# Kernel tuning notes

Measured on AMD Instinct MI355X. Metric: run time of the kernel, lower is better.

## Reference

```python
import jax, jax.numpy as jnp
import numpy as np

P_DROP = 0.2
NEG_SLOPE = 0.2


def setup_inputs() -> dict:
    key = jax.random.key(0)
    ks = jax.random.split(key, 12)
    N, E = 50000, 800000
    IN, H1, H2, OUT = 256, 256, 128, 64
    x = jax.random.normal(ks[0], (N, IN), dtype=jnp.float32)
    adj_rows = jax.random.randint(ks[1], (E,), 0, N, dtype=jnp.int32)
    adj_cols = jax.random.randint(ks[2], (E,), 0, N, dtype=jnp.int32)
    adj_vals = jax.random.uniform(ks[3], (E,), dtype=jnp.float32)
    W1 = jax.random.normal(ks[4], (H1, IN), dtype=jnp.float32) * (1.0 / np.sqrt(IN))
    b1 = jax.random.normal(ks[5], (H1,), dtype=jnp.float32) * 0.01
    W2 = jax.random.normal(ks[6], (H2, H1), dtype=jnp.float32) * (1.0 / np.sqrt(H1))
    b2 = jax.random.normal(ks[7], (H2,), dtype=jnp.float32) * 0.01
    W3 = jax.random.normal(ks[8], (OUT, H2), dtype=jnp.float32) * (1.0 / np.sqrt(H2))
    b3 = jax.random.normal(ks[9], (OUT,), dtype=jnp.float32) * 0.01
    mask1 = jax.random.bernoulli(ks[10], 1.0 - P_DROP, (N, H1))
    mask2 = jax.random.bernoulli(ks[11], 1.0 - P_DROP, (N, H2))
    return {"x": x, "adj_rows": adj_rows, "adj_cols": adj_cols, "adj_vals": adj_vals,
            "W1": W1, "b1": b1, "W2": W2, "b2": b2, "W3": W3, "b3": b3,
            "mask1": mask1, "mask2": mask2}


def _spmm(rows, cols, vals, h, n_nodes):
    # sparse adjacency matmul: out[r] = sum_e vals[e] * h[cols[e]] for rows[e]==r
    msgs = vals[:, None] * h[cols]  # [E, d] irregular gather
    return jax.ops.segment_sum(msgs, rows, num_segments=n_nodes)


def _gcn_layer(x, W, b, rows, cols, vals, n_nodes):
    h = x @ W.T + b  # nn.Linear
    return _spmm(rows, cols, vals, h, n_nodes)


def reference(x, adj_rows, adj_cols, adj_vals, W1, b1, W2, b2, W3, b3, mask1, mask2):
    N = x.shape[0]
    keep = 1.0 / (1.0 - P_DROP)
    h = _gcn_layer(x, W1, b1, adj_rows, adj_cols, adj_vals, N)
    h = jnp.where(h >= 0, h, NEG_SLOPE * h)
    h = jnp.where(mask1, h * keep, 0.0)
    h = _gcn_layer(h, W2, b2, adj_rows, adj_cols, adj_vals, N)
    h = jnp.where(h >= 0, h, NEG_SLOPE * h)
    h = jnp.where(mask2, h * keep, 0.0)
    z = _gcn_layer(h, W3, b3, adj_rows, adj_cols, adj_vals, N)
    return z
```

## Files before the change

kernel.cpp:

```cpp
#include <hip/hip_runtime.h>


typedef unsigned short ushort_t;
typedef __attribute__((ext_vector_type(8))) short bf16x8;
typedef __attribute__((ext_vector_type(4))) float f32x4;
typedef __attribute__((ext_vector_type(2))) unsigned int u32x2;

__device__ __forceinline__ float bf2f(ushort_t u) {
  return __uint_as_float(((unsigned int)u) << 16);
}
__device__ __forceinline__ ushort_t f2bf(float f) {
  unsigned int u = __float_as_uint(f);
  return (ushort_t)((u + 0x7FFFu + ((u >> 16) & 1u)) >> 16);
}
__device__ __forceinline__ float read_f(const void* p, int fm, size_t i) {
  return fm ? bf2f(((const ushort_t*)p)[i]) : ((const float*)p)[i];
}

__device__ __forceinline__ size_t frag_off(int m, int k, int K) {
  return (size_t)(m >> 4) * 16 * K + ((size_t)(k >> 5) << 9) +
         (((k >> 3) & 3) << 7) + ((m & 15) << 3) + (k & 7);
}

__device__ __forceinline__ bool mask_keep(const void* mask, int mm, size_t o) {
  switch (mm) {
    case 1:  return ((const int*)mask)[o] != 0;
    case 2:  return ((const unsigned int*)mask)[o] != 0u;
    case 3:  return ((const ushort_t*)mask)[o] != 0;
    default: return ((const unsigned char*)mask)[o] != 0;
  }
}

__global__ void prep_kernel(const void* __restrict__ x,
                            const void* __restrict__ m1,
                            const void* __restrict__ m2,
                            int* __restrict__ modes,
                            int* __restrict__ zero_region, int zn) {
  if (blockIdx.x == 0) {
    __shared__ int bfok;
    if (threadIdx.x == 0) bfok = 1;
    __syncthreads();
    for (int i = threadIdx.x; i < 8192; i += blockDim.x) {
      ushort_t h = ((const ushort_t*)x)[i];
      int e = (h >> 7) & 0xFF;
      if (!(h == 0 || (e >= 95 && e <= 133))) atomicAnd(&bfok, 0);
    }
    __syncthreads();
    if (threadIdx.x == 0) modes[0] = bfok;
  } else if (blockIdx.x <= 2) {
    const void* p = (blockIdx.x == 1) ? m1 : m2;
    __shared__ int ok[4];
    if (threadIdx.x < 4) ok[threadIdx.x] = 1;
    __syncthreads();
    for (int i = threadIdx.x; i < 4096; i += blockDim.x) {
      unsigned int w = ((const unsigned int*)p)[i];
      if (!(w == 0u || w == 1u)) atomicAnd(&ok[0], 0);
      if (!(w == 0u || w == 0x3F800000u)) atomicAnd(&ok[1], 0);
      unsigned int h16 = w >> 16, l16 = w & 0xFFFFu;
      if (!((h16 == 0u || h16 == 0x3F80u) && (l16 == 0u || l16 == 0x3F80u)))
        atomicAnd(&ok[2], 0);
      if (((w | (w >> 8) | (w >> 16) | (w >> 24)) & 0xFEu) != 0u) atomicAnd(&ok[3], 0);
    }
    __syncthreads();
    if (threadIdx.x == 0)
      modes[blockIdx.x] = ok[0] ? 1 : (ok[1] ? 2 : (ok[2] ? 3 : 0));
  } else {
    int i = (blockIdx.x - 3) * blockDim.x + threadIdx.x;
    int stride = (gridDim.x - 3) * blockDim.x;
    for (; i < zn; i += stride) zero_region[i] = 0;
  }
}

__global__ void hist_kernel(const int* __restrict__ rows, int* __restrict__ cnt, int E) {
  int i = blockIdx.x * blockDim.x + threadIdx.x;
  int stride = gridDim.x * blockDim.x;
  for (; i < E; i += stride) atomicAdd(&cnt[rows[i]], 1);
}

__global__ void scan_part_kernel(const int* __restrict__ cnt, int* __restrict__ part, int n) {
  __shared__ int s[256];
  int i = blockIdx.x * 256 + threadIdx.x;
  s[threadIdx.x] = (i < n) ? cnt[i] : 0;
  __syncthreads();
  for (int off = 128; off > 0; off >>= 1) {
    if (threadIdx.x < off) s[threadIdx.x] += s[threadIdx.x + off];
    __syncthreads();
  }
  if (threadIdx.x == 0) part[blockIdx.x] = s[0];
}

__global__ __launch_bounds__(1024) void scan_top_kernel(int* __restrict__ part, int P) {
  __shared__ int s[1024];
  int t = threadIdx.x;
  int v = (t < P) ? part[t] : 0;
  s[t] = v;
  __syncthreads();
  for (int off = 1; off < 1024; off <<= 1) {
    int x = s[t];
    int y = (t >= off) ? s[t - off] : 0;
    __syncthreads();
    s[t] = x + y;
    __syncthreads();
  }
  if (t < P) part[t] = s[t] - v;
}

__global__ void scan_apply_kernel(const int* __restrict__ cnt, const int* __restrict__ part,
                                  int* __restrict__ row_start, int n) {
  __shared__ int s[256];
  int base = part[blockIdx.x];
  int i = blockIdx.x * 256 + threadIdx.x;
  int v = (i < n) ? cnt[i] : 0;
  s[threadIdx.x] = v;
  __syncthreads();
  for (int off = 1; off < 256; off <<= 1) {
    int x = s[threadIdx.x];
    int y = (threadIdx.x >= off) ? s[threadIdx.x - off] : 0;
    __syncthreads();
    s[threadIdx.x] = x + y;
    __syncthreads();
  }
  if (i < n) row_start[i] = base + s[threadIdx.x] - v;
  if (i == n - 1) row_start[n] = base + s[threadIdx.x];
}

__global__ void scatter_kernel(const int* __restrict__ rows, const int* __restrict__ cols,
                               const void* __restrict__ vals, const int* __restrict__ fm_p,
                               const int* __restrict__ row_start, int* __restrict__ fill,
                               int2* __restrict__ ecv, int E) {
  int fm = *fm_p;
  int i = blockIdx.x * blockDim.x + threadIdx.x;
  int stride = gridDim.x * blockDim.x;
  for (; i < E; i += stride) {
    int r = rows[i];
    int pos = atomicAdd(&fill[r], 1);
    int idx = row_start[r] + pos;
    ecv[idx] = make_int2(cols[i], __float_as_int(read_f(vals, fm, i)));
  }
}

__global__ void convert_all_kernel(
    const void* __restrict__ W1, const void* __restrict__ W2, const void* __restrict__ W3,
    const void* __restrict__ b1, const void* __restrict__ b2, const void* __restrict__ b3,
    const void* __restrict__ x, const int* __restrict__ fm_p,
    ushort_t* __restrict__ whi, ushort_t* __restrict__ wlo,
    float* __restrict__ biasf, ushort_t* __restrict__ xbf,
    int n1, int n2, int n3, int h1, int h2, int h3, int K1, int K2, int K3, int nx) {
  int fm = *fm_p;
  int wtot = n1 + n2 + n3;
  int btot = h1 + h2 + h3;
  int nx4 = nx / 4;
  int total = wtot + btot + nx4;
  int i = blockIdx.x * blockDim.x + threadIdx.x;
  int stride = gridDim.x * blockDim.x;
  for (; i < total; i += stride) {
    if (i < wtot) {
      const void* src; int j, K; size_t base;
      if (i < n1) { src = W1; j = i; K = K1; base = 0; }
      else if (i < n1 + n2) { src = W2; j = i - n1; K = K2; base = n1; }
      else { src = W3; j = i - n1 - n2; K = K3; base = (size_t)n1 + n2; }
      int n = j / K, k = j - n * K;
      float v = read_f(src, fm, j);
      ushort_t h = f2bf(v);
      size_t o = base + frag_off(n, k, K);
      whi[o] = h;
      wlo[o] = f2bf(v - bf2f(h));
    } else if (i < wtot + btot) {
      int k = i - wtot;
      const void* src; int j;
      if (k < h1) { src = b1; j = k; }
      else if (k < h1 + h2) { src = b2; j = k - h1; }
      else { src = b3; j = k - h1 - h2; }
      biasf[k] = read_f(src, fm, j);
    } else {
      int k4 = i - wtot - btot;
      int m = k4 / (K1 / 4);
      int k0 = (k4 - m * (K1 / 4)) * 4;
      ushort_t p0, p1, p2, p3;
      if (fm == 0) {
        f32x4 v = ((const f32x4*)x)[k4];
        p0 = f2bf(v[0]); p1 = f2bf(v[1]); p2 = f2bf(v[2]); p3 = f2bf(v[3]);
      } else {
        const ushort_t* xb = (const ushort_t*)x + (size_t)k4 * 4;
        p0 = xb[0]; p1 = xb[1]; p2 = xb[2]; p3 = xb[3];
      }
      size_t o = frag_off(m, k0, K1);
      *(u32x2*)(xbf + o) = (u32x2){
          (unsigned int)p0 | ((unsigned int)p1 << 16),
          (unsigned int)p2 | ((unsigned int)p3 << 16)};
    }
  }
}

template<int KC>
__global__ __launch_bounds__(256) void gemm_breg_kernel(
    const ushort_t* __restrict__ A,
    const ushort_t* __restrict__ Whi, const ushort_t* __restrict__ Wlo,
    const float* __restrict__ bias, ushort_t* __restrict__ g, int ldg,
    int M, int nct) {
  const int K = KC * 32;
  int wave = threadIdx.x >> 6, lane = threadIdx.x & 63;
  int gw = blockIdx.x * 4 + wave;
  int NW = gridDim.x * 4;
  int mr = lane & 15, quad = lane >> 4;
  int ct = gw % nct;
  int nrt = (M + 15) >> 4;
  int ntasks = nct * nrt;
  if (gw >= ntasks) return;

  bf16x8 wh[KC], wl[KC];
  {
    const ushort_t* wp = Whi + (size_t)ct * 16 * K + lane * 8;
    const ushort_t* wq = Wlo + (size_t)ct * 16 * K + lane * 8;
#pragma unroll
    for (int kc = 0; kc < KC; ++kc) {
      wh[kc] = *(const bf16x8*)(wp + kc * 512);
      wl[kc] = *(const bf16x8*)(wq + kc * 512);
    }
  }
  int col = ct * 16 + mr;
  float bv = bias[col];

  int task = gw;
  bf16x8 af[KC];
  {
    const ushort_t* ap = A + (size_t)(task / nct) * 16 * K + lane * 8;
#pragma unroll
    for (int kc = 0; kc < KC; ++kc) af[kc] = *(const bf16x8*)(ap + kc * 512);
  }

#pragma unroll 1
  for (;;) {
    int next = task + NW;
    bool has_next = next < ntasks;
    bf16x8 afn[KC];
    if (has_next) {
      const ushort_t* ap = A + (size_t)(next / nct) * 16 * K + lane * 8;
#pragma unroll
      for (int kc = 0; kc < KC; ++kc) afn[kc] = *(const bf16x8*)(ap + kc * 512);
    }

    f32x4 acc[4];
#pragma unroll
    for (int t = 0; t < 4; ++t) acc[t] = (f32x4){0.f, 0.f, 0.f, 0.f};
#pragma unroll
    for (int kc = 0; kc < KC; ++kc) {
      acc[(2 * kc) & 3] = __builtin_amdgcn_mfma_f32_16x16x32_bf16(af[kc], wh[kc], acc[(2 * kc) & 3], 0, 0, 0);
      acc[(2 * kc + 1) & 3] = __builtin_amdgcn_mfma_f32_16x16x32_bf16(af[kc], wl[kc], acc[(2 * kc + 1) & 3], 0, 0, 0);
    }
    int m0 = (task / nct) * 16;
#pragma unroll
    for (int r = 0; r < 4; ++r) {
      int row = m0 + quad * 4 + r;
      float s = ((acc[0][r] + acc[1][r]) + (acc[2][r] + acc[3][r])) + bv;
      if (row < M) g[(size_t)row * ldg + col] = f2bf(s);
    }
    if (!has_next) break;
#pragma unroll
    for (int kc = 0; kc < KC; ++kc) af[kc] = afn[kc];
    task = next;
  }
}

template<int MODE, int VEC>
__global__ __launch_bounds__(256) void spmm7_kernel(
    const int* __restrict__ row_start, const int2* __restrict__ ecv,
    const ushort_t* __restrict__ G, int D,
    const void* __restrict__ mask, const int* __restrict__ mmode_p,
    void* __restrict__ outp, int N) {
  int wave = threadIdx.x >> 6, lane = threadIdx.x & 63;
  int r = blockIdx.x * 4 + wave;
  if (r >= N) return;
  int f0 = lane * VEC;
  int e  = __builtin_amdgcn_readfirstlane(row_start[r]);
  int e1 = __builtin_amdgcn_readfirstlane(row_start[r + 1]);
  float a[VEC];
#pragma unroll
  for (int q = 0; q < VEC; ++q) a[q] = 0.f;

  for (; e + 8 <= e1; e += 8) {
    int2 cv[8];
#pragma unroll
    for (int j = 0; j < 8; ++j) cv[j] = ecv[e + j];
    if (VEC == 4) {
      u32x2 gg[8];
#pragma unroll
      for (int j = 0; j < 8; ++j)
        gg[j] = *(const u32x2*)(G + (size_t)cv[j].x * D + f0);
#pragma unroll
      for (int j = 0; j < 8; ++j) {
        float v = __int_as_float(cv[j].y);
        a[0] += v * bf2f((ushort_t)gg[j][0]);
        a[1] += v * bf2f((ushort_t)(gg[j][0] >> 16));
        a[2] += v * bf2f((ushort_t)gg[j][1]);
        a[3] += v * bf2f((ushort_t)(gg[j][1] >> 16));
      }
    } else if (VEC == 2) {
      unsigned int gg[8];
#pragma unroll
      for (int j = 0; j < 8; ++j)
        gg[j] = *(const unsigned int*)(G + (size_t)cv[j].x * D + f0);
#pragma unroll
      for (int j = 0; j < 8; ++j) {
        float v = __int_as_float(cv[j].y);
        a[0] += v * bf2f((ushort_t)gg[j]);
        a[1] += v * bf2f((ushort_t)(gg[j] >> 16));
      }
    } else {
      ushort_t h[8];
#pragma unroll
      for (int j = 0; j < 8; ++j) h[j] = G[(size_t)cv[j].x * D + f0];
#pragma unroll
      for (int j = 0; j < 8; ++j) a[0] += __int_as_float(cv[j].y) * bf2f(h[j]);
    }
  }
  if (e < e1) {
    int idx[8]; float v[8];
#pragma unroll
    for (int j = 0; j < 8; ++j) {
      int ee = e + j;
      bool ok = ee < e1;
      int2 cv = ecv[ok ? ee : e1 - 1];
      idx[j] = cv.x;
      v[j] = ok ? __int_as_float(cv.y) : 0.f;
    }
    if (VEC == 4) {
      u32x2 gg[8];
#pragma unroll
      for (int j = 0; j < 8; ++j)
        gg[j] = *(const u32x2*)(G + (size_t)idx[j] * D + f0);
#pragma unroll
      for (int j = 0; j < 8; ++j) {
        a[0] += v[j] * bf2f((ushort_t)gg[j][0]);
        a[1] += v[j] * bf2f((ushort_t)(gg[j][0] >> 16));
        a[2] += v[j] * bf2f((ushort_t)gg[j][1]);
        a[3] += v[j] * bf2f((ushort_t)(gg[j][1] >> 16));
      }
    } else if (VEC == 2) {
      unsigned int gg[8];
#pragma unroll
      for (int j = 0; j < 8; ++j)
        gg[j] = *(const unsigned int*)(G + (size_t)idx[j] * D + f0);
#pragma unroll
      for (int j = 0; j < 8; ++j) {
        a[0] += v[j] * bf2f((ushort_t)gg[j]);
        a[1] += v[j] * bf2f((ushort_t)(gg[j] >> 16));
      }
    } else {
      ushort_t h[8];
#pragma unroll
      for (int j = 0; j < 8; ++j) h[j] = G[(size_t)idx[j] * D + f0];
#pragma unroll
      for (int j = 0; j < 8; ++j) a[0] += v[j] * bf2f(h[j]);
    }
  }

  if (MODE == 1) {
    size_t om = (size_t)r * D + f0;
    int mm = *mmode_p;
    ushort_t pk[VEC];
#pragma unroll
    for (int q = 0; q < VEC; ++q) {
      float t = a[q];
      t = (t >= 0.f) ? t : 0.2f * t;
      t = mask_keep(mask, mm, om + q) ? t * 1.25f : 0.f;
      pk[q] = f2bf(t);
    }
    size_t o = frag_off(r, f0, D);
    if (VEC == 4) {
      *(u32x2*)((ushort_t*)outp + o) = (u32x2){
          (unsigned int)pk[0] | ((unsigned int)pk[1] << 16),
          (unsigned int)pk[2] | ((unsigned int)pk[3] << 16)};
    } else if (VEC == 2) {
      *(unsigned int*)((ushort_t*)outp + o) =
          (unsigned int)pk[0] | ((unsigned int)pk[1] << 16);
    } else {
      ((ushort_t*)outp)[o] = pk[0];
    }
  } else {
    size_t o = (size_t)r * D + f0;
#pragma unroll
    for (int q = 0; q < VEC; ++q) ((float*)outp)[o + q] = a[q];
  }
}

extern "C" void kernel_launch(void* const* d_in, const int* in_sizes, int n_in,
                              void* d_out, int out_size, void* d_ws, size_t ws_size,
                              hipStream_t stream) {
  const void* x     = d_in[0];
  const int*  rows  = (const int*)d_in[1];
  const int*  cols  = (const int*)d_in[2];
  const void* vals  = d_in[3];
  const void* W1    = d_in[4];
  const void* b1    = d_in[5];
  const void* W2    = d_in[6];
  const void* b2    = d_in[7];
  const void* W3    = d_in[8];
  const void* b3    = d_in[9];
  const void* mask1 = d_in[10];
  const void* mask2 = d_in[11];

  const int H1  = in_sizes[5];
  const int H2  = in_sizes[7];
  const int OUT = in_sizes[9];
  const int IN  = in_sizes[4] / H1;
  const int N   = in_sizes[0] / IN;
  const int E   = in_sizes[1];
  const int W1n = in_sizes[4], W2n = in_sizes[6], W3n = in_sizes[8];
  const int Np  = ((N + 15) / 16) * 16;

  char* ws = (char*)d_ws;
  size_t off = 0;
  auto alloc = [&](size_t bytes) -> void* {
    void* p = ws + off;
    off = (off + bytes + 255) & ~(size_t)255;
    return p;
  };
  int*      modes     = (int*)alloc(4 * 4);
  int*      row_start = (int*)alloc((size_t)(N + 1) * 4);
  int*      cnt       = (int*)alloc((size_t)N * 8);
  int*      part      = (int*)alloc(1024 * 4);
  int2*     ecv       = (int2*)alloc((size_t)E * 8);
  ushort_t* whi       = (ushort_t*)alloc((size_t)(W1n + W2n + W3n) * 2);
  ushort_t* wlo       = (ushort_t*)alloc((size_t)(W1n + W2n + W3n) * 2);
  float*    biasf     = (float*)alloc((size_t)(H1 + H2 + OUT) * 4);
  ushort_t* bufA      = (ushort_t*)alloc((size_t)Np * H1 * 2);
  ushort_t* bufB      = (ushort_t*)alloc((size_t)Np * H1 * 2);
  ushort_t* bufC      = (ushort_t*)alloc((size_t)Np * H1 * 2);

  int* fmode = modes;
  int* mm1   = modes + 1;
  int* mm2   = modes + 2;
  int* fill  = cnt + N;
  ushort_t* w1hi = whi,             *w1lo = wlo;
  ushort_t* w2hi = whi + W1n,       *w2lo = wlo + W1n;
  ushort_t* w3hi = whi + W1n + W2n, *w3lo = wlo + W1n + W2n;

  prep_kernel<<<259, 256, 0, stream>>>(x, mask1, mask2, modes, cnt, 2 * N);

  const int P = (N + 255) / 256;
  hist_kernel<<<1024, 256, 0, stream>>>(rows, cnt, E);
  scan_part_kernel<<<P, 256, 0, stream>>>(cnt, part, N);
  scan_top_kernel<<<1, 1024, 0, stream>>>(part, P);
  scan_apply_kernel<<<P, 256, 0, stream>>>(cnt, part, row_start, N);
  scatter_kernel<<<1024, 256, 0, stream>>>(rows, cols, vals, fmode, row_start, fill, ecv, E);

  convert_all_kernel<<<2048, 256, 0, stream>>>(
      W1, W2, W3, b1, b2, b3, x, fmode, whi, wlo, biasf, bufA,
      W1n, W2n, W3n, H1, H2, OUT, IN, H1, H2, N * IN);

  const int GEMM_BLOCKS = 1024;
  int spmm_grid = (N + 3) / 4;

  gemm_breg_kernel<8><<<GEMM_BLOCKS, 256, 0, stream>>>(
      bufA, w1hi, w1lo, biasf, bufB, H1, N, H1 / 16);
  spmm7_kernel<1, 4><<<spmm_grid, 256, 0, stream>>>(
      row_start, ecv, bufB, H1, mask1, mm1, bufC, N);
  gemm_breg_kernel<8><<<GEMM_BLOCKS, 256, 0, stream>>>(
      bufC, w2hi, w2lo, biasf + H1, bufB, H2, N, H2 / 16);
  spmm7_kernel<1, 2><<<spmm_grid, 256, 0, stream>>>(
      row_start, ecv, bufB, H2, mask2, mm2, bufA, N);
  gemm_breg_kernel<4><<<GEMM_BLOCKS, 256, 0, stream>>>(
      bufA, w3hi, w3lo, biasf + H1 + H2, bufB, OUT, N, OUT / 16);
  spmm7_kernel<0, 1><<<spmm_grid, 256, 0, stream>>>(
      row_start, ecv, bufB, OUT, nullptr, fmode, d_out, N);
}
```

Measured before the change: 454.0 us.

## Merge scatter and convert kernels; vectorize mask loads and stage SpMM fragment stores

```diff
diff --git a/kernel.cpp b/kernel.cpp
--- a/kernel.cpp
+++ b/kernel.cpp
@@ -5,6 +5,7 @@
 typedef __attribute__((ext_vector_type(8))) short bf16x8;
 typedef __attribute__((ext_vector_type(4))) float f32x4;
 typedef __attribute__((ext_vector_type(2))) unsigned int u32x2;
+typedef __attribute__((ext_vector_type(4))) unsigned int u32x4;
 
 __device__ __forceinline__ float bf2f(ushort_t u) {
   return __uint_as_float(((unsigned int)u) << 16);
@@ -124,70 +125,70 @@
   if (i == n - 1) row_start[n] = base + s[threadIdx.x];
 }
 
-__global__ void scatter_kernel(const int* __restrict__ rows, const int* __restrict__ cols,
-                               const void* __restrict__ vals, const int* __restrict__ fm_p,
-                               const int* __restrict__ row_start, int* __restrict__ fill,
-                               int2* __restrict__ ecv, int E) {
-  int fm = *fm_p;
-  int i = blockIdx.x * blockDim.x + threadIdx.x;
-  int stride = gridDim.x * blockDim.x;
-  for (; i < E; i += stride) {
-    int r = rows[i];
-    int pos = atomicAdd(&fill[r], 1);
-    int idx = row_start[r] + pos;
-    ecv[idx] = make_int2(cols[i], __float_as_int(read_f(vals, fm, i)));
-  }
-}
-
-__global__ void convert_all_kernel(
+__global__ void scatter_convert_kernel(
+    const int* __restrict__ rows, const int* __restrict__ cols,
+    const void* __restrict__ vals, const int* __restrict__ fm_p,
+    const int* __restrict__ row_start, int* __restrict__ fill,
+    int2* __restrict__ ecv, int E,
     const void* __restrict__ W1, const void* __restrict__ W2, const void* __restrict__ W3,
     const void* __restrict__ b1, const void* __restrict__ b2, const void* __restrict__ b3,
-    const void* __restrict__ x, const int* __restrict__ fm_p,
+    const void* __restrict__ x,
     ushort_t* __restrict__ whi, ushort_t* __restrict__ wlo,
     float* __restrict__ biasf, ushort_t* __restrict__ xbf,
     int n1, int n2, int n3, int h1, int h2, int h3, int K1, int K2, int K3, int nx) {
   int fm = *fm_p;
-  int wtot = n1 + n2 + n3;
-  int btot = h1 + h2 + h3;
-  int nx4 = nx / 4;
-  int total = wtot + btot + nx4;
-  int i = blockIdx.x * blockDim.x + threadIdx.x;
-  int stride = gridDim.x * blockDim.x;
-  for (; i < total; i += stride) {
-    if (i < wtot) {
-      const void* src; int j, K; size_t base;
-      if (i < n1) { src = W1; j = i; K = K1; base = 0; }
-      else if (i < n1 + n2) { src = W2; j = i - n1; K = K2; base = n1; }
-      else { src = W3; j = i - n1 - n2; K = K3; base = (size_t)n1 + n2; }
-      int n = j / K, k = j - n * K;
-      float v = read_f(src, fm, j);
-      ushort_t h = f2bf(v);
-      size_t o = base + frag_off(n, k, K);
-      whi[o] = h;
-      wlo[o] = f2bf(v - bf2f(h));
-    } else if (i < wtot + btot) {
-      int k = i - wtot;
-      const void* src; int j;
-      if (k < h1) { src = b1; j = k; }
-      else if (k < h1 + h2) { src = b2; j = k - h1; }
-      else { src = b3; j = k - h1 - h2; }
-      biasf[k] = read_f(src, fm, j);
-    } else {
-      int k4 = i - wtot - btot;
-      int m = k4 / (K1 / 4);
-      int k0 = (k4 - m * (K1 / 4)) * 4;
-      ushort_t p0, p1, p2, p3;
-      if (fm == 0) {
-        f32x4 v = ((const f32x4*)x)[k4];
-        p0 = f2bf(v[0]); p1 = f2bf(v[1]); p2 = f2bf(v[2]); p3 = f2bf(v[3]);
+  if (blockIdx.x < 1024) {
+    int i = blockIdx.x * blockDim.x + threadIdx.x;
+    int stride = 1024 * blockDim.x;
+    for (; i < E; i += stride) {
+      int r = rows[i];
+      int pos = atomicAdd(&fill[r], 1);
+      int idx = row_start[r] + pos;
+      ecv[idx] = make_int2(cols[i], __float_as_int(read_f(vals, fm, i)));
+    }
+  } else {
+    int wtot = n1 + n2 + n3;
+    int btot = h1 + h2 + h3;
+    int nx4 = nx / 4;
+    int total = wtot + btot + nx4;
+    int i = (blockIdx.x - 1024) * blockDim.x + threadIdx.x;
+    int stride = (gridDim.x - 1024) * blockDim.x;
+    for (; i < total; i += stride) {
+      if (i < wtot) {
+        const void* src; int j, K; size_t base;
+        if (i < n1) { src = W1; j = i; K = K1; base = 0; }
+        else if (i < n1 + n2) { src = W2; j = i - n1; K = K2; base = n1; }
+        else { src = W3; j = i - n1 - n2; K = K3; base = (size_t)n1 + n2; }
+        int n = j / K, k = j - n * K;
+        float v = read_f(src, fm, j);
+        ushort_t h = f2bf(v);
+        size_t o = base + frag_off(n, k, K);
+        whi[o] = h;
+        wlo[o] = f2bf(v - bf2f(h));
+      } else if (i < wtot + btot) {
+        int k = i - wtot;
+        const void* src; int j;
+        if (k < h1) { src = b1; j = k; }
+        else if (k < h1 + h2) { src = b2; j = k - h1; }
+        else { src = b3; j = k - h1 - h2; }
+        biasf[k] = read_f(src, fm, j);
       } else {
-        const ushort_t* xb = (const ushort_t*)x + (size_t)k4 * 4;
-        p0 = xb[0]; p1 = xb[1]; p2 = xb[2]; p3 = xb[3];
-      }
-      size_t o = frag_off(m, k0, K1);
-      *(u32x2*)(xbf + o) = (u32x2){
-          (unsigned int)p0 | ((unsigned int)p1 << 16),
-          (unsigned int)p2 | ((unsigned int)p3 << 16)};
+        int k4 = i - wtot - btot;
+        int m = k4 / (K1 / 4);
+        int k0 = (k4 - m * (K1 / 4)) * 4;
+        ushort_t p0, p1, p2, p3;
+        if (fm == 0) {
+          f32x4 v = ((const f32x4*)x)[k4];
+          p0 = f2bf(v[0]); p1 = f2bf(v[1]); p2 = f2bf(v[2]); p3 = f2bf(v[3]);
+        } else {
+          const ushort_t* xb = (const ushort_t*)x + (size_t)k4 * 4;
+          p0 = xb[0]; p1 = xb[1]; p2 = xb[2]; p3 = xb[3];
+        }
+        size_t o = frag_off(m, k0, K1);
+        *(u32x2*)(xbf + o) = (u32x2){
+            (unsigned int)p0 | ((unsigned int)p1 << 16),
+            (unsigned int)p2 | ((unsigned int)p3 << 16)};
+      }
     }
   }
 }
@@ -263,124 +264,149 @@
 }
 
 template<int MODE, int VEC>
-__global__ __launch_bounds__(256) void spmm7_kernel(
+__global__ __launch_bounds__(256) void spmm8_kernel(
     const int* __restrict__ row_start, const int2* __restrict__ ecv,
     const ushort_t* __restrict__ G, int D,
     const void* __restrict__ mask, const int* __restrict__ mmode_p,
     void* __restrict__ outp, int N) {
+  __shared__ ushort_t stage[1024];
   int wave = threadIdx.x >> 6, lane = threadIdx.x & 63;
   int r = blockIdx.x * 4 + wave;
-  if (r >= N) return;
+  bool active = r < N;
+  float a[VEC];
+#pragma unroll
+  for (int q = 0; q < VEC; ++q) a[q] = 0.f;
   int f0 = lane * VEC;
-  int e  = __builtin_amdgcn_readfirstlane(row_start[r]);
-  int e1 = __builtin_amdgcn_readfirstlane(row_start[r + 1]);
-  float a[VEC];
-#pragma unroll
-  for (int q = 0; q < VEC; ++q) a[q] = 0.f;
-
-  for (; e + 8 <= e1; e += 8) {
-    int2 cv[8];
-#pragma unroll
-    for (int j = 0; j < 8; ++j) cv[j] = ecv[e + j];
-    if (VEC == 4) {
-      u32x2 gg[8];
-#pragma unroll
-      for (int j = 0; j < 8; ++j)
-        gg[j] = *(const u32x2*)(G + (size_t)cv[j].x * D + f0);
+
+  if (active) {
+    int e  = __builtin_amdgcn_readfirstlane(row_start[r]);
+    int e1 = __builtin_amdgcn_readfirstlane(row_start[r + 1]);
+    for (; e + 8 <= e1; e += 8) {
+      int2 cv[8];
+#pragma unroll
+      for (int j = 0; j < 8; ++j) cv[j] = ecv[e + j];
+      if (VEC == 4) {
+        u32x2 gg[8];
+#pragma unroll
+        for (int j = 0; j < 8; ++j)
+          gg[j] = *(const u32x2*)(G + (size_t)cv[j].x * D + f0);
+#pragma unroll
+        for (int j = 0; j < 8; ++j) {
+          float v = __int_as_float(cv[j].y);
+          a[0] += v * bf2f((ushort_t)gg[j][0]);
+          a[1] += v * bf2f((ushort_t)(gg[j][0] >> 16));
+          a[2] += v * bf2f((ushort_t)gg[j][1]);
+          a[3] += v * bf2f((ushort_t)(gg[j][1] >> 16));
+        }
+      } else if (VEC == 2) {
+        unsigned int gg[8];
+#pragma unroll
+        for (int j = 0; j < 8; ++j)
+          gg[j] = *(const unsigned int*)(G + (size_t)cv[j].x * D + f0);
+#pragma unroll
+        for (int j = 0; j < 8; ++j) {
+          float v = __int_as_float(cv[j].y);
+          a[0] += v * bf2f((ushort_t)gg[j]);
+          a[1] += v * bf2f((ushort_t)(gg[j] >> 16));
+        }
+      } else {
+        ushort_t h[8];
+#pragma unroll
+        for (int j = 0; j < 8; ++j) h[j] = G[(size_t)cv[j].x * D + f0];
+#pragma unroll
+        for (int j = 0; j < 8; ++j) a[0] += __int_as_float(cv[j].y) * bf2f(h[j]);
+      }
+    }
+    if (e < e1) {
+      int idx[8]; float v[8];
 #pragma unroll
       for (int j = 0; j < 8; ++j) {
-        float v = __int_as_float(cv[j].y);
-        a[0] += v * bf2f((ushort_t)gg[j][0]);
-        a[1] += v * bf2f((ushort_t)(gg[j][0] >> 16));
-        a[2] += v * bf2f((ushort_t)gg[j][1]);
-        a[3] += v * bf2f((ushort_t)(gg[j][1] >> 16));
-      }
-    } else if (VEC == 2) {
-      unsigned int gg[8];
-#pragma unroll
-      for (int j = 0; j < 8; ++j)
-        gg[j] = *(const unsigned int*)(G + (size_t)cv[j].x * D + f0);
-#pragma unroll
-      for (int j = 0; j < 8; ++j) {
-        float v = __int_as_float(cv[j].y);
-        a[0] += v * bf2f((ushort_t)gg[j]);
-        a[1] += v * bf2f((ushort_t)(gg[j] >> 16));
-      }
-    } else {
-      ushort_t h[8];
-#pragma unroll
-      for (int j = 0; j < 8; ++j) h[j] = G[(size_t)cv[j].x * D + f0];
-#pragma unroll
-      for (int j = 0; j < 8; ++j) a[0] += __int_as_float(cv[j].y) * bf2f(h[j]);
-    }
-  }
-  if (e < e1) {
-    int idx[8]; float v[8];
-#pragma unroll
-    for (int j = 0; j < 8; ++j) {
-      int ee = e + j;
-      bool ok = ee < e1;
-      int2 cv = ecv[ok ? ee : e1 - 1];
-      idx[j] = cv.x;
-      v[j] = ok ? __int_as_float(cv.y) : 0.f;
-    }
-    if (VEC == 4) {
-      u32x2 gg[8];
-#pragma unroll
-      for (int j = 0; j < 8; ++j)
-        gg[j] = *(const u32x2*)(G + (size_t)idx[j] * D + f0);
-#pragma unroll
-      for (int j = 0; j < 8; ++j) {
-        a[0] += v[j] * bf2f((ushort_t)gg[j][0]);
-        a[1] += v[j] * bf2f((ushort_t)(gg[j][0] >> 16));
-        a[2] += v[j] * bf2f((ushort_t)gg[j][1]);
-        a[3] += v[j] * bf2f((ushort_t)(gg[j][1] >> 16));
-      }
-    } else if (VEC == 2) {
-      unsigned int gg[8];
-#pragma unroll
-      for (int j = 0; j < 8; ++j)
-        gg[j] = *(const unsigned int*)(G + (size_t)idx[j] * D + f0);
-#pragma unroll
-      for (int j = 0; j < 8; ++j) {
-        a[0] += v[j] * bf2f((ushort_t)gg[j]);
-        a[1] += v[j] * bf2f((ushort_t)(gg[j] >> 16));
-      }
-    } else {
-      ushort_t h[8];
-#pragma unroll
-      for (int j = 0; j < 8; ++j) h[j] = G[(size_t)idx[j] * D + f0];
-#pragma unroll
-      for (int j = 0; j < 8; ++j) a[0] += v[j] * bf2f(h[j]);
+        int ee = e + j;
+        bool ok = ee < e1;
+        int2 cv = ecv[ok ? ee : e1 - 1];
+        idx[j] = cv.x;
+        v[j] = ok ? __int_as_float(cv.y) : 0.f;
+      }
+      if (VEC == 4) {
+        u32x2 gg[8];
+#pragma unroll
+        for (int j = 0; j < 8; ++j)
+          gg[j] = *(const u32x2*)(G + (size_t)idx[j] * D + f0);
+#pragma unroll
+        for (int j = 0; j < 8; ++j) {
+          a[0] += v[j] * bf2f((ushort_t)gg[j][0]);
+          a[1] += v[j] * bf2f((ushort_t)(gg[j][0] >> 16));
+          a[2] += v[j] * bf2f((ushort_t)gg[j][1]);
+          a[3] += v[j] * bf2f((ushort_t)(gg[j][1] >> 16));
+        }
+      } else if (VEC == 2) {
+        unsigned int gg[8];
+#pragma unroll
+        for (int j = 0; j < 8; ++j)
+          gg[j] = *(const unsigned int*)(G + (size_t)idx[j] * D + f0);
+#pragma unroll
+        for (int j = 0; j < 8; ++j) {
+          a[0] += v[j] * bf2f((ushort_t)gg[j]);
+          a[1] += v[j] * bf2f((ushort_t)(gg[j] >> 16));
+        }
+      } else {
+        ushort_t h[8];
+#pragma unroll
+        for (int j = 0; j < 8; ++j) h[j] = G[(size_t)idx[j] * D + f0];
+#pragma unroll
+        for (int j = 0; j < 8; ++j) a[0] += v[j] * bf2f(h[j]);
+      }
     }
   }
 
   if (MODE == 1) {
-    size_t om = (size_t)r * D + f0;
-    int mm = *mmode_p;
-    ushort_t pk[VEC];
-#pragma unroll
-    for (int q = 0; q < VEC; ++q) {
-      float t = a[q];
-      t = (t >= 0.f) ? t : 0.2f * t;
-      t = mask_keep(mask, mm, om + q) ? t * 1.25f : 0.f;
-      pk[q] = f2bf(t);
-    }
-    size_t o = frag_off(r, f0, D);
-    if (VEC == 4) {
-      *(u32x2*)((ushort_t*)outp + o) = (u32x2){
-          (unsigned int)pk[0] | ((unsigned int)pk[1] << 16),
-          (unsigned int)pk[2] | ((unsigned int)pk[3] << 16)};
-    } else if (VEC == 2) {
-      *(unsigned int*)((ushort_t*)outp + o) =
-          (unsigned int)pk[0] | ((unsigned int)pk[1] << 16);
-    } else {
-      ((ushort_t*)outp)[o] = pk[0];
+    if (active) {
+      size_t om = (size_t)r * D + f0;
+      int mm = *mmode_p;
+      bool keep[VEC];
+      if (mm == 1 || mm == 2) {
+        if (VEC == 4) {
+          u32x4 mv = *(const u32x4*)((const unsigned int*)mask + om);
+#pragma unroll
+          for (int q = 0; q < VEC; ++q) keep[q] = mv[q] != 0u;
+        } else if (VEC == 2) {
+          u32x2 mv = *(const u32x2*)((const unsigned int*)mask + om);
+#pragma unroll
+          for (int q = 0; q < VEC; ++q) keep[q] = mv[q] != 0u;
+        } else {
+          keep[0] = ((const unsigned int*)mask)[om] != 0u;
+        }
+      } else {
+#pragma unroll
+        for (int q = 0; q < VEC; ++q) keep[q] = mask_keep(mask, mm, om + q);
+      }
+#pragma unroll
+      for (int q = 0; q < VEC; ++q) {
+        float t = a[q];
+        t = (t >= 0.f) ? t : 0.2f * t;
+        t = keep[q] ? t * 1.25f : 0.f;
+        stage[wave * D + f0 + q] = f2bf(t);
+      }
+    }
+    __syncthreads();
+    if (threadIdx.x < D) {
+      int g = threadIdx.x >> 3, s = threadIdx.x & 7;
+      int kc = g >> 2, quad = g & 3;
+      int sr = s >> 1;
+      int r0 = blockIdx.x * 4;
+      if (r0 + sr < N) {
+        int kk = kc * 32 + quad * 8 + (s & 1) * 4;
+        size_t dst = (size_t)(r0 >> 4) * 16 * D + ((size_t)kc << 9) +
+                     (quad << 7) + ((r0 & 15) << 3) + s * 4;
+        *(u32x2*)((ushort_t*)outp + dst) = *(const u32x2*)(stage + sr * D + kk);
+      }
     }
   } else {
-    size_t o = (size_t)r * D + f0;
-#pragma unroll
-    for (int q = 0; q < VEC; ++q) ((float*)outp)[o + q] = a[q];
+    if (active) {
+      size_t o = (size_t)r * D + f0;
+#pragma unroll
+      for (int q = 0; q < VEC; ++q) ((float*)outp)[o + q] = a[q];
+    }
   }
 }
 
@@ -443,10 +469,10 @@
   scan_part_kernel<<<P, 256, 0, stream>>>(cnt, part, N);
   scan_top_kernel<<<1, 1024, 0, stream>>>(part, P);
   scan_apply_kernel<<<P, 256, 0, stream>>>(cnt, part, row_start, N);
-  scatter_kernel<<<1024, 256, 0, stream>>>(rows, cols, vals, fmode, row_start, fill, ecv, E);
-
-  convert_all_kernel<<<2048, 256, 0, stream>>>(
-      W1, W2, W3, b1, b2, b3, x, fmode, whi, wlo, biasf, bufA,
+
+  scatter_convert_kernel<<<3072, 256, 0, stream>>>(
+      rows, cols, vals, fmode, row_start, fill, ecv, E,
+      W1, W2, W3, b1, b2, b3, x, whi, wlo, biasf, bufA,
       W1n, W2n, W3n, H1, H2, OUT, IN, H1, H2, N * IN);
 
   const int GEMM_BLOCKS = 1024;
@@ -454,14 +480,14 @@
 
   gemm_breg_kernel<8><<<GEMM_BLOCKS, 256, 0, stream>>>(
       bufA, w1hi, w1lo, biasf, bufB, H1, N, H1 / 16);
-  spmm7_kernel<1, 4><<<spmm_grid, 256, 0, stream>>>(
+  spmm8_kernel<1, 4><<<spmm_grid, 256, 0, stream>>>(
       row_start, ecv, bufB, H1, mask1, mm1, bufC, N);
   gemm_breg_kernel<8><<<GEMM_BLOCKS, 256, 0, stream>>>(
       bufC, w2hi, w2lo, biasf + H1, bufB, H2, N, H2 / 16);
-  spmm7_kernel<1, 2><<<spmm_grid, 256, 0, stream>>>(
+  spmm8_kernel<1, 2><<<spmm_grid, 256, 0, stream>>>(
       row_start, ecv, bufB, H2, mask2, mm2, bufA, N);
   gemm_breg_kernel<4><<<GEMM_BLOCKS, 256, 0, stream>>>(
       bufA, w3hi, w3lo, biasf + H1 + H2, bufB, OUT, N, OUT / 16);
-  spmm7_kernel<0, 1><<<spmm_grid, 256, 0, stream>>>(
+  spmm8_kernel<0, 1><<<spmm_grid, 256, 0, stream>>>(
       row_start, ecv, bufB, OUT, nullptr, fmode, d_out, N);
 }
```

After: 439.4 us. 3.2% less time.
